# Kernel tuning notes

Measured on AMD Instinct MI355X. Metric: run time of the kernel, lower is better.

## Reference

```python
import jax, jax.numpy as jnp
import numpy as np

H = 256          # hidden_size
L = 2            # num_layers
K = 4            # khops
R = 128          # relation_num
N_NODES = 20000
N_EDGES = 160000
N_LG_EDGES = 640000


def setup_inputs() -> dict:
    key = jax.random.key(0)
    ks = iter(jax.random.split(key, 40))
    def nrm(shape, s=1.0):
        return jax.random.normal(next(ks), shape, dtype=jnp.float32) * s
    w = 1.0 / float(np.sqrt(H))
    return {
        "x": nrm((N_NODES, H)),
        "edge_feat": jax.random.randint(next(ks), (N_EDGES,), 0, R),
        "edge_index_g": jax.random.randint(next(ks), (2, N_EDGES), 0, N_NODES),
        "edge_index_lg": jax.random.randint(next(ks), (2, N_LG_EDGES), 0, N_EDGES),
        "rel_embed": nrm((R, H)),
        # per-layer, per-core (0=node update, 1=edge update) parameter stacks
        "w_self": nrm((L, 2, H, H), w), "b_self": jnp.zeros((L, 2, H), jnp.float32),
        "w_khop": nrm((L, 2, K, H, H), w), "b_khop": jnp.zeros((L, 2, K, H), jnp.float32),
        "w_fuse": nrm((L, 2, H, H), w), "b_fuse": jnp.zeros((L, 2, H), jnp.float32),
        "w_ff1": nrm((L, 2, H, 4 * H), w), "b_ff1": jnp.zeros((L, 2, 4 * H), jnp.float32),
        "w_ff2": nrm((L, 2, 4 * H, H), 1.0 / float(np.sqrt(4 * H))), "b_ff2": jnp.zeros((L, 2, H), jnp.float32),
        "ln1_g": jnp.ones((L, 2, H), jnp.float32), "ln1_b": jnp.zeros((L, 2, H), jnp.float32),
        "ln2_g": jnp.ones((L, 2, H), jnp.float32), "ln2_b": jnp.zeros((L, 2, H), jnp.float32),
    }


def _layernorm(x, g, b, eps=1e-5):
    m = jnp.mean(x, axis=-1, keepdims=True)
    v = jnp.var(x, axis=-1, keepdims=True)
    return (x - m) * jax.lax.rsqrt(v + eps) * g + b


def _core(p, src, dst, x, fused):
    """LGNNCore.forward (eval mode, dropout never applied in core)."""
    (ws, bs, wk, bk, wf, bf, w1, b1, w2, b2, g1, c1, g2, c2) = p
    n = x.shape[0]
    prev = x @ ws + bs
    # k-hop copy_src + sum aggregation, each hop gets its own linear
    z = x
    kh = jnp.zeros_like(prev)
    for i in range(wk.shape[0]):
        z = jax.ops.segment_sum(z[src], dst, num_segments=n)
        kh = kh + z @ wk[i] + bk[i]
    edge = fused @ wf + bf
    out = jax.nn.gelu(prev + kh + edge, approximate=False)
    out = _layernorm(x + out, g1, c1)
    ffn = jax.nn.gelu(out @ w1 + b1, approximate=False) @ w2 + b2
    return _layernorm(out + ffn, g2, c2)


def reference(x, edge_feat, edge_index_g, edge_index_lg, rel_embed,
              w_self, b_self, w_khop, b_khop, w_fuse, b_fuse,
              w_ff1, b_ff1, w_ff2, b_ff2, ln1_g, ln1_b, ln2_g, ln2_b):
    lg_x = rel_embed[edge_feat]                       # [n_edges, H]
    src_g, dst_g = edge_index_g[0], edge_index_g[1]
    src_l, dst_l = edge_index_lg[0], edge_index_lg[1]
    n_nodes = x.shape[0]
    for l in range(w_self.shape[0]):
        def pick(c):
            return (w_self[l, c], b_self[l, c], w_khop[l, c], b_khop[l, c],
                    w_fuse[l, c], b_fuse[l, c], w_ff1[l, c], b_ff1[l, c],
                    w_ff2[l, c], b_ff2[l, c], ln1_g[l, c], ln1_b[l, c],
                    ln2_g[l, c], ln2_b[l, c])
        # pmpd @ lg_x : scatter each edge feature to both of its endpoints
        fused_nodes = (jax.ops.segment_sum(lg_x, src_g, num_segments=n_nodes)
                       + jax.ops.segment_sum(lg_x, dst_g, num_segments=n_nodes))
        # pmpd^T @ x : gather both endpoint node features per edge
        fused_edges = x[src_g] + x[dst_g]
        new_x = _core(pick(0), src_g, dst_g, x, fused_nodes)
        new_lg_x = _core(pick(1), src_l, dst_l, lg_x, fused_edges)
        x, lg_x = new_x, new_lg_x
    return x, lg_x
```

## Files before the change

### kernel.cpp

```cpp
#include <hip/hip_runtime.h>

typedef __bf16 bf16;
typedef __attribute__((ext_vector_type(8))) __bf16 bf16x8;
typedef __attribute__((ext_vector_type(4))) __bf16 bf16x4;
typedef __attribute__((ext_vector_type(4))) float f32x4;

#define HD 256
#define GEMM_GELU 2

__device__ __forceinline__ float gelu_f(float x) {
  float x2 = x * x;
  float u = 1.5957691216057308f * x * fmaf(0.044715f, x2, 1.0f);
  float e = __expf(-u);
  return x / (1.0f + e);
}

__device__ __forceinline__ void gload_lds16(const void* g, void* l) {
  __builtin_amdgcn_global_load_lds(
      (const __attribute__((address_space(1))) unsigned int*)g,
      (__attribute__((address_space(3))) unsigned int*)l, 16, 0, 0);
}

__global__ __launch_bounds__(256) void gemm_k(
    const bf16* __restrict__ A, const bf16* __restrict__ Wt,
    const float* __restrict__ bias, bf16* __restrict__ C,
    int M, int Kd, int lda, int ldc, int flags)
{
  __shared__ __align__(16) bf16 sA[128 * 32];
  __shared__ __align__(16) bf16 sB[128 * 32];
  const int t = threadIdx.x;
  const int lane = t & 63, w = t >> 6;
  const int n0 = blockIdx.x * 128, m0 = blockIdx.y * 128;
  const int wr = w >> 1, wc = w & 1;
  const int lm = lane & 15, quad = lane >> 4;

  const int srow = t >> 2;
  const int cg = (t & 3) ^ ((t >> 3) & 3);
  const bool full = (m0 + 128 <= M);

  const char* a0 = (const char*)(A + (size_t)(m0 + srow) * lda) + cg * 16;
  const char* a1 = (const char*)(A + (size_t)(m0 + srow + 64) * lda) + cg * 16;
  const char* b0 = (const char*)(Wt + (size_t)(n0 + srow) * Kd) + cg * 16;
  const char* b1 = (const char*)(Wt + (size_t)(n0 + srow + 64) * Kd) + cg * 16;
  bf16* lA0 = sA + w * 512;
  bf16* lA1 = sA + 2048 + w * 512;
  bf16* lB0 = sB + w * 512;
  bf16* lB1 = sB + 2048 + w * 512;

  const int soff = (quad ^ ((lm >> 1) & 3)) * 8;

  f32x4 acc[4][4];
#pragma unroll
  for (int i = 0; i < 4; i++)
#pragma unroll
    for (int j = 0; j < 4; j++)
#pragma unroll
      for (int r = 0; r < 4; r++) acc[i][j][r] = 0.f;

  for (int kb = 0; kb < Kd; kb += 32) {
    size_t ko = (size_t)kb * 2;
    if (full) {
      gload_lds16(a0 + ko, lA0);
      gload_lds16(a1 + ko, lA1);
    } else {
#pragma unroll
      for (int c = 0; c < 2; c++) {
        int row = srow + c * 64;
        int gr = m0 + row;
        bf16x8 va;
#pragma unroll
        for (int q = 0; q < 8; q++) va[q] = (bf16)0.f;
        if (gr < M) va = *(const bf16x8*)((const char*)(A + (size_t)gr * lda) + ko + cg * 16);
        *(bf16x8*)(sA + row * 32 + (t & 3) * 8) = va;
      }
    }
    gload_lds16(b0 + ko, lB0);
    gload_lds16(b1 + ko, lB1);
    __syncthreads();
    bf16x8 af[4], bv[4];
#pragma unroll
    for (int i = 0; i < 4; i++) af[i] = *(const bf16x8*)(sA + (wr * 64 + i * 16 + lm) * 32 + soff);
#pragma unroll
    for (int j = 0; j < 4; j++) bv[j] = *(const bf16x8*)(sB + (wc * 64 + j * 16 + lm) * 32 + soff);
#pragma unroll
    for (int i = 0; i < 4; i++)
#pragma unroll
      for (int j = 0; j < 4; j++)
        acc[i][j] = __builtin_amdgcn_mfma_f32_16x16x32_bf16(bv[j], af[i], acc[i][j], 0, 0, 0);
    __syncthreads();
  }
#pragma unroll
  for (int i = 0; i < 4; i++) {
    int gr = m0 + wr * 64 + i * 16 + lm;
    if (gr < M) {
      bf16* crow = C + (size_t)gr * ldc;
#pragma unroll
      for (int j = 0; j < 4; j++) {
        int gc = n0 + wc * 64 + j * 16 + quad * 4;
        float4 bia = *(const float4*)(bias + gc);
        float v0 = acc[i][j][0] + bia.x;
        float v1 = acc[i][j][1] + bia.y;
        float v2 = acc[i][j][2] + bia.z;
        float v3 = acc[i][j][3] + bia.w;
        if (flags & GEMM_GELU) {
          v0 = gelu_f(v0); v1 = gelu_f(v1); v2 = gelu_f(v2); v3 = gelu_f(v3);
        }
        bf16x4 o = {(bf16)v0, (bf16)v1, (bf16)v2, (bf16)v3};
        *(bf16x4*)(crow + gc) = o;
      }
    }
  }
}

__global__ __launch_bounds__(256) void segsum_k(
    const int* __restrict__ offs, const int* __restrict__ cols,
    const bf16* __restrict__ in, int ldin, bf16* __restrict__ out, int ldout, int nseg)
{
  int wid = threadIdx.x >> 6, lane = threadIdx.x & 63;
  int seg = blockIdx.x * 4 + wid;
  if (seg >= nseg) return;
  int b = offs[seg], e = offs[seg + 1];
  float a0 = 0.f, a1 = 0.f, a2 = 0.f, a3 = 0.f;
  for (int i = b; i < e; i++) {
    int c = cols[i];
    bf16x4 v = *(const bf16x4*)(in + (size_t)c * ldin + lane * 4);
    a0 += (float)v.x; a1 += (float)v.y; a2 += (float)v.z; a3 += (float)v.w;
  }
  bf16x4 o = {(bf16)a0, (bf16)a1, (bf16)a2, (bf16)a3};
  *(bf16x4*)(out + (size_t)seg * ldout + lane * 4) = o;
}

__global__ __launch_bounds__(256) void ln_k(
    const bf16* __restrict__ X, int ldx, const bf16* __restrict__ A,
    const float* __restrict__ gam, const float* __restrict__ bet,
    bf16* __restrict__ outb, float* __restrict__ outf, int M, int apply_gelu)
{
  int wid = threadIdx.x >> 6, lane = threadIdx.x & 63;
  int row = blockIdx.x * 4 + wid;
  if (row >= M) return;
  size_t xbase = (size_t)row * ldx + lane * 4;
  size_t abase = (size_t)row * HD + lane * 4;
  bf16x4 xv = *(const bf16x4*)(X + xbase);
  bf16x4 av = *(const bf16x4*)(A + abase);
  float s0, s1, s2, s3;
  if (apply_gelu) {
    s0 = (float)xv.x + gelu_f((float)av.x);
    s1 = (float)xv.y + gelu_f((float)av.y);
    s2 = (float)xv.z + gelu_f((float)av.z);
    s3 = (float)xv.w + gelu_f((float)av.w);
  } else {
    s0 = (float)xv.x + (float)av.x;
    s1 = (float)xv.y + (float)av.y;
    s2 = (float)xv.z + (float)av.z;
    s3 = (float)xv.w + (float)av.w;
  }
  float sum = s0 + s1 + s2 + s3;
#pragma unroll
  for (int o = 32; o; o >>= 1) sum += __shfl_xor(sum, o, 64);
  float mean = sum * (1.0f / 256.0f);
  float d0 = s0 - mean, d1 = s1 - mean, d2 = s2 - mean, d3 = s3 - mean;
  float vs = d0 * d0 + d1 * d1 + d2 * d2 + d3 * d3;
#pragma unroll
  for (int o = 32; o; o >>= 1) vs += __shfl_xor(vs, o, 64);
  float rstd = rsqrtf(vs * (1.0f / 256.0f) + 1e-5f);
  float4 g = *(const float4*)(gam + lane * 4);
  float4 bb = *(const float4*)(bet + lane * 4);
  float y0 = d0 * rstd * g.x + bb.x;
  float y1 = d1 * rstd * g.y + bb.y;
  float y2 = d2 * rstd * g.z + bb.z;
  float y3 = d3 * rstd * g.w + bb.w;
  if (outb) {
    bf16x4 o = {(bf16)y0, (bf16)y1, (bf16)y2, (bf16)y3};
    *(bf16x4*)(outb + xbase) = o;
  }
  if (outf) {
    float4 o = {y0, y1, y2, y3};
    *(float4*)(outf + abase) = o;
  }
}

__global__ __launch_bounds__(256) void gather_rel_k(
    const int* __restrict__ feat, const float* __restrict__ rel,
    bf16* __restrict__ out, int ldout, int NE)
{
  int wid = threadIdx.x >> 6, lane = threadIdx.x & 63;
  int e = blockIdx.x * 4 + wid;
  if (e >= NE) return;
  int f = feat[e];
  float4 v = *(const float4*)(rel + (size_t)f * HD + lane * 4);
  bf16x4 o = {(bf16)v.x, (bf16)v.y, (bf16)v.z, (bf16)v.w};
  *(bf16x4*)(out + (size_t)e * ldout + lane * 4) = o;
}

__global__ __launch_bounds__(256) void gather2_k(
    const int* __restrict__ src, const int* __restrict__ dst,
    const bf16* __restrict__ x, int ldx, bf16* __restrict__ out, int ldout, int NE)
{
  int wid = threadIdx.x >> 6, lane = threadIdx.x & 63;
  int e = blockIdx.x * 4 + wid;
  if (e >= NE) return;
  int s = src[e], d = dst[e];
  bf16x4 a = *(const bf16x4*)(x + (size_t)s * ldx + lane * 4);
  bf16x4 b = *(const bf16x4*)(x + (size_t)d * ldx + lane * 4);
  bf16x4 o = {(bf16)((float)a.x + (float)b.x), (bf16)((float)a.y + (float)b.y),
              (bf16)((float)a.z + (float)b.z), (bf16)((float)a.w + (float)b.w)};
  *(bf16x4*)(out + (size_t)e * ldout + lane * 4) = o;
}

__global__ __launch_bounds__(256) void f2b_k(const float* __restrict__ in,
                                             bf16* __restrict__ out, int ldout, int M) {
  int wid = threadIdx.x >> 6, lane = threadIdx.x & 63;
  int row = blockIdx.x * 4 + wid;
  if (row >= M) return;
  float4 v = *(const float4*)(in + (size_t)row * HD + lane * 4);
  bf16x4 o = {(bf16)v.x, (bf16)v.y, (bf16)v.z, (bf16)v.w};
  *(bf16x4*)(out + (size_t)row * ldout + lane * 4) = o;
}

__global__ __launch_bounds__(256) void wtrans_k(const float* __restrict__ in, bf16* __restrict__ out,
                                                int Kd, int Nd) {
  size_t moff = (size_t)blockIdx.y * Kd * Nd;
  int id = blockIdx.x * 256 + threadIdx.x;
  if (id >= Kd * Nd) return;
  int n = id / Kd, k = id - n * Kd;
  out[moff + id] = (bf16)in[moff + (size_t)k * Nd + n];
}

__global__ __launch_bounds__(256) void wcat_k(const float* __restrict__ ws, const float* __restrict__ wk,
                                              const float* __restrict__ wf, bf16* __restrict__ out,
                                              int KH, int CW) {
  int mi = blockIdx.y;
  int id = blockIdx.x * 256 + threadIdx.x;
  if (id >= HD * CW) return;
  int n = id / CW, k = id - n * CW;
  int s = k >> 8, kk = k & 255;
  float v;
  if (s == 0)       v = ws[((size_t)mi * HD + kk) * HD + n];
  else if (s <= KH) v = wk[(((size_t)mi * KH + (s - 1)) * HD + kk) * HD + n];
  else              v = wf[((size_t)mi * HD + kk) * HD + n];
  out[(size_t)mi * HD * CW + id] = (bf16)v;
}

__global__ __launch_bounds__(256) void bcat_k(const float* __restrict__ bs, const float* __restrict__ bk,
                                              const float* __restrict__ bf, float* __restrict__ out, int KH) {
  int mi = blockIdx.x, n = threadIdx.x;
  float v = bs[(size_t)mi * HD + n] + bf[(size_t)mi * HD + n];
  for (int i = 0; i < KH; i++) v += bk[((size_t)mi * KH + i) * HD + n];
  out[(size_t)mi * HD + n] = v;
}

__global__ __launch_bounds__(256) void count_k(const int* __restrict__ keys, int n, int* __restrict__ cnt) {
  int i = blockIdx.x * 256 + threadIdx.x;
  if (i < n) atomicAdd(&cnt[keys[i]], 1);
}
__global__ __launch_bounds__(256) void scan1_k(const int* __restrict__ in, int* __restrict__ out,
                                               int* __restrict__ bsum, int n) {
  __shared__ int sh[256];
  int t = threadIdx.x;
  int i0 = blockIdx.x * 1024 + t * 4;
  int v0 = (i0 < n) ? in[i0] : 0;
  int v1 = (i0 + 1 < n) ? in[i0 + 1] : 0;
  int v2 = (i0 + 2 < n) ? in[i0 + 2] : 0;
  int v3 = (i0 + 3 < n) ? in[i0 + 3] : 0;
  int tsum = v0 + v1 + v2 + v3;
  sh[t] = tsum;
  __syncthreads();
  for (int o = 1; o < 256; o <<= 1) {
    int x = (t >= o) ? sh[t - o] : 0;
    __syncthreads();
    sh[t] += x;
    __syncthreads();
  }
  int e0 = sh[t] - tsum;
  if (t == 255) bsum[blockIdx.x] = sh[255];
  if (i0 < n) out[i0] = e0;
  e0 += v0;
  if (i0 + 1 < n) out[i0 + 1] = e0;
  e0 += v1;
  if (i0 + 2 < n) out[i0 + 2] = e0;
  e0 += v2;
  if (i0 + 3 < n) out[i0 + 3] = e0;
}
__global__ void scan2_k(int* bsum, int nb, int* total) {
  if (threadIdx.x == 0 && blockIdx.x == 0) {
    int acc = 0;
    for (int i = 0; i < nb; i++) { int v = bsum[i]; bsum[i] = acc; acc += v; }
    *total = acc;
  }
}
__global__ __launch_bounds__(256) void scan3_k(int* out, const int* bsum, int n) {
  int i = blockIdx.x * 256 + threadIdx.x;
  if (i < n) out[i] += bsum[i >> 10];
}
__global__ __launch_bounds__(256) void fill_k(const int* __restrict__ keys, const int* __restrict__ vals,
                                              int n, int modE, int* __restrict__ cursor, int* __restrict__ cols) {
  int i = blockIdx.x * 256 + threadIdx.x;
  if (i >= n) return;
  int pos = atomicAdd(&cursor[keys[i]], 1);
  cols[pos] = vals ? vals[i] : (i < modE ? i : i - modE);
}

extern "C" void kernel_launch(void* const* d_in, const int* in_sizes, int n_in,
                              void* d_out, int out_size, void* d_ws, size_t ws_size,
                              hipStream_t stream)
{
  const float* x_in      = (const float*)d_in[0];
  const int*   edge_feat = (const int*)d_in[1];
  const int*   eig       = (const int*)d_in[2];
  const int*   eil       = (const int*)d_in[3];
  const float* rel       = (const float*)d_in[4];
  const float* w_self = (const float*)d_in[5];
  const float* b_self = (const float*)d_in[6];
  const float* w_khop = (const float*)d_in[7];
  const float* b_khop = (const float*)d_in[8];
  const float* w_fuse = (const float*)d_in[9];
  const float* b_fuse = (const float*)d_in[10];
  const float* w_ff1  = (const float*)d_in[11];
  const float* b_ff1  = (const float*)d_in[12];
  const float* w_ff2  = (const float*)d_in[13];
  const float* b_ff2  = (const float*)d_in[14];
  const float* ln1_g  = (const float*)d_in[15];
  const float* ln1_b  = (const float*)d_in[16];
  const float* ln2_g  = (const float*)d_in[17];
  const float* ln2_b  = (const float*)d_in[18];

  const int NN = in_sizes[0] / HD;
  const int NE = in_sizes[1];
  const int NL = in_sizes[3] / 2;
  const int L  = in_sizes[5] / (2 * HD * HD);
  const int KH = in_sizes[7] / (L * 2 * HD * HD);
  const int CW = (KH + 2) * HD;

  char* p = (char*)d_ws;
  auto alloc = [&](size_t bytes) -> void* {
    void* r = (void*)p;
    p += (bytes + 255) & ~(size_t)255;
    return r;
  };

  bf16* n_cat  = (bf16*)alloc((size_t)NN * CW * 2);
  bf16* lg_cat = (bf16*)alloc((size_t)NE * CW * 2);
  bf16* acc_n  = (bf16*)alloc((size_t)NN * HD * 2);
  bf16* acc_e  = (bf16*)alloc((size_t)NE * HD * 2);

  bf16*  wcat_t = (bf16*)alloc((size_t)L * 2 * HD * CW * 2);
  float* bcat   = (float*)alloc((size_t)L * 2 * HD * 4);
  bf16*  wff1_t = (bf16*)alloc((size_t)L * 2 * HD * 4 * HD * 2);
  bf16*  wff2_t = (bf16*)alloc((size_t)L * 2 * HD * 4 * HD * 2);

  int* inc_offs = (int*)alloc((size_t)(NN + 1) * 4);
  int* inc_cur  = (int*)alloc((size_t)NN * 4);
  int* inc_cols = (int*)alloc((size_t)2 * NE * 4);
  int* ng_offs  = (int*)alloc((size_t)(NN + 1) * 4);
  int* ng_cur   = (int*)alloc((size_t)NN * 4);
  int* ng_cols  = (int*)alloc((size_t)NE * 4);
  int* lg_offs  = (int*)alloc((size_t)(NE + 1) * 4);
  int* lg_cur   = (int*)alloc((size_t)NE * 4);
  int* lg_cols  = (int*)alloc((size_t)NL * 4);
  int* bsum     = (int*)alloc(3 * 256 * 4);

  wcat_k<<<dim3((HD * CW + 255) / 256, L * 2), 256, 0, stream>>>(w_self, w_khop, w_fuse, wcat_t, KH, CW);
  bcat_k<<<L * 2, 256, 0, stream>>>(b_self, b_khop, b_fuse, bcat, KH);
  wtrans_k<<<dim3((HD * 4 * HD + 255) / 256, L * 2), 256, 0, stream>>>(w_ff1, wff1_t, HD, 4 * HD);
  wtrans_k<<<dim3((HD * 4 * HD + 255) / 256, L * 2), 256, 0, stream>>>(w_ff2, wff2_t, 4 * HD, HD);

  f2b_k<<<(NN + 3) / 4, 256, 0, stream>>>(x_in, n_cat, CW, NN);
  gather_rel_k<<<(NE + 3) / 4, 256, 0, stream>>>(edge_feat, rel, lg_cat, CW, NE);

  auto build_csr = [&](const int* keys, int nkeys, const int* vals, int modE,
                       int nseg, int* offs, int* cur, int* cols, int* bs) {
    int nb = (nseg + 1023) / 1024;
    hipMemsetAsync(offs, 0, (size_t)(nseg + 1) * 4, stream);
    count_k<<<(nkeys + 255) / 256, 256, 0, stream>>>(keys, nkeys, offs);
    scan1_k<<<nb, 256, 0, stream>>>(offs, offs, bs, nseg);
    scan2_k<<<1, 1, 0, stream>>>(bs, nb, offs + nseg);
    scan3_k<<<(nseg + 255) / 256, 256, 0, stream>>>(offs, bs, nseg);
    hipMemcpyAsync(cur, offs, (size_t)nseg * 4, hipMemcpyDeviceToDevice, stream);
    fill_k<<<(nkeys + 255) / 256, 256, 0, stream>>>(keys, vals, nkeys, modE, cur, cols);
  };
  build_csr(eig, 2 * NE, nullptr, NE, NN, inc_offs, inc_cur, inc_cols, bsum);
  build_csr(eig + NE, NE, eig, 0, NN, ng_offs, ng_cur, ng_cols, bsum + 256);
  build_csr(eil + NL, NL, eil, 0, NE, lg_offs, lg_cur, lg_cols, bsum + 512);

  float* out_x  = (float*)d_out;
  float* out_lg = (float*)d_out + (size_t)NN * HD;

  auto run_core = [&](bf16* cat, bf16* accb, const int* coffs, const int* ccols,
                      int M, int l, int c, float* outf) {
    size_t mi = (size_t)(l * 2 + c);
    int mb = (M + 127) / 128;
    for (int i = 1; i <= KH; i++)
      segsum_k<<<(M + 3) / 4, 256, 0, stream>>>(coffs, ccols, cat + (size_t)(i - 1) * HD, CW,
                                                cat + (size_t)i * HD, CW, M);
    gemm_k<<<dim3(2, mb), 256, 0, stream>>>(cat, wcat_t + mi * HD * CW, bcat + mi * HD,
                                            accb, M, CW, CW, HD, 0);
    ln_k<<<(M + 3) / 4, 256, 0, stream>>>(cat, CW, accb, ln1_g + mi * HD, ln1_b + mi * HD,
                                          cat, (float*)nullptr, M, 1);
    bf16* hid = cat + HD;
    int FC = (M > 40000) ? 40000 : M;
    for (int c0 = 0; c0 < M; c0 += FC) {
      int mc = (M - c0 < FC) ? (M - c0) : FC;
      int mbc = (mc + 127) / 128;
      gemm_k<<<dim3(8, mbc), 256, 0, stream>>>(cat + (size_t)c0 * CW, wff1_t + mi * HD * 4 * HD,
                                               b_ff1 + mi * 4 * HD, hid, mc, HD, CW, CW, GEMM_GELU);
      gemm_k<<<dim3(2, mbc), 256, 0, stream>>>(hid, wff2_t + mi * 4 * HD * HD, b_ff2 + mi * HD,
                                               accb + (size_t)c0 * HD, mc, 4 * HD, CW, HD, 0);
    }
    ln_k<<<(M + 3) / 4, 256, 0, stream>>>(cat, CW, accb, ln2_g + mi * HD, ln2_b + mi * HD,
                                          cat, outf, M, 0);
  };

  for (int l = 0; l < L; l++) {
    segsum_k<<<(NN + 3) / 4, 256, 0, stream>>>(inc_offs, inc_cols, lg_cat, CW,
                                               n_cat + (size_t)(KH + 1) * HD, CW, NN);
    gather2_k<<<(NE + 3) / 4, 256, 0, stream>>>(eig, eig + NE, n_cat, CW,
                                                lg_cat + (size_t)(KH + 1) * HD, CW, NE);
    run_core(n_cat, acc_n, ng_offs, ng_cols, NN, l, 0, (l == L - 1) ? out_x : nullptr);
    run_core(lg_cat, acc_e, lg_offs, lg_cols, NE, l, 1, (l == L - 1) ? out_lg : nullptr);
  }
}
```

Measured before the change: 3.329 ms.

## Double-buffer GEMM LDS tiles to overlap global loads with MFMA

The GEMM kernel gets two LDS buffers for A and B. The next k-tile is issued into the spare buffer while MFMAs run on the current one, so there is one barrier per iteration instead of two. Bias loads are hoisted out of the row loop in the epilogue. This doubles LDS use to 32 KB per block, which may lower occupancy, and correctness now depends on the global_load_lds writes being waited for before the barrier.

```diff
diff --git a/kernel.cpp b/kernel.cpp
--- a/kernel.cpp
+++ b/kernel.cpp
@@ -26,8 +26,8 @@
     const float* __restrict__ bias, bf16* __restrict__ C,
     int M, int Kd, int lda, int ldc, int flags)
 {
-  __shared__ __align__(16) bf16 sA[128 * 32];
-  __shared__ __align__(16) bf16 sB[128 * 32];
+  __shared__ __align__(16) bf16 sA[2][128 * 32];
+  __shared__ __align__(16) bf16 sB[2][128 * 32];
   const int t = threadIdx.x;
   const int lane = t & 63, w = t >> 6;
   const int n0 = blockIdx.x * 128, m0 = blockIdx.y * 128;
@@ -41,11 +41,7 @@
   const char* a0 = (const char*)(A + (size_t)(m0 + srow) * lda) + cg * 16;
   const char* a1 = (const char*)(A + (size_t)(m0 + srow + 64) * lda) + cg * 16;
   const char* b0 = (const char*)(Wt + (size_t)(n0 + srow) * Kd) + cg * 16;
-  const char* b1 = (const char*)(Wt + (size_t)(n0 + srow + 64) * Kd) + cg * 16;
-  bf16* lA0 = sA + w * 512;
-  bf16* lA1 = sA + 2048 + w * 512;
-  bf16* lB0 = sB + w * 512;
-  bf16* lB1 = sB + 2048 + w * 512;
+  const char* b1 = (const char*)(Wt + (size_t)(n0 + srow) * Kd) + (size_t)64 * Kd * 2 + cg * 16;
 
   const int soff = (quad ^ ((lm >> 1) & 3)) * 8;
 
@@ -57,11 +53,15 @@
 #pragma unroll
       for (int r = 0; r < 4; r++) acc[i][j][r] = 0.f;
 
-  for (int kb = 0; kb < Kd; kb += 32) {
+  const int nk = Kd >> 5;
+
+  auto stage = [&](int buf, int kb) {
     size_t ko = (size_t)kb * 2;
+    bf16* SA = sA[buf];
+    bf16* SB = sB[buf];
     if (full) {
-      gload_lds16(a0 + ko, lA0);
-      gload_lds16(a1 + ko, lA1);
+      gload_lds16(a0 + ko, SA + w * 512);
+      gload_lds16(a1 + ko, SA + 2048 + w * 512);
     } else {
 #pragma unroll
       for (int c = 0; c < 2; c++) {
@@ -71,24 +71,43 @@
 #pragma unroll
         for (int q = 0; q < 8; q++) va[q] = (bf16)0.f;
         if (gr < M) va = *(const bf16x8*)((const char*)(A + (size_t)gr * lda) + ko + cg * 16);
-        *(bf16x8*)(sA + row * 32 + (t & 3) * 8) = va;
+        *(bf16x8*)(SA + row * 32 + (t & 3) * 8) = va;
       }
     }
-    gload_lds16(b0 + ko, lB0);
-    gload_lds16(b1 + ko, lB1);
-    __syncthreads();
+    gload_lds16(b0 + ko, SB + w * 512);
+    gload_lds16(b1 + ko, SB + 2048 + w * 512);
+  };
+
+  auto compute = [&](int buf) {
+    const bf16* SA = sA[buf];
+    const bf16* SB = sB[buf];
     bf16x8 af[4], bv[4];
 #pragma unroll
-    for (int i = 0; i < 4; i++) af[i] = *(const bf16x8*)(sA + (wr * 64 + i * 16 + lm) * 32 + soff);
-#pragma unroll
-    for (int j = 0; j < 4; j++) bv[j] = *(const bf16x8*)(sB + (wc * 64 + j * 16 + lm) * 32 + soff);
+    for (int i = 0; i < 4; i++) af[i] = *(const bf16x8*)(SA + (wr * 64 + i * 16 + lm) * 32 + soff);
+#pragma unroll
+    for (int j = 0; j < 4; j++) bv[j] = *(const bf16x8*)(SB + (wc * 64 + j * 16 + lm) * 32 + soff);
 #pragma unroll
     for (int i = 0; i < 4; i++)
 #pragma unroll
       for (int j = 0; j < 4; j++)
         acc[i][j] = __builtin_amdgcn_mfma_f32_16x16x32_bf16(bv[j], af[i], acc[i][j], 0, 0, 0);
+  };
+
+  stage(0, 0);
+  __syncthreads();
+  int cur = 0;
+  for (int kt = 0; kt < nk - 1; ++kt) {
+    stage(cur ^ 1, (kt + 1) << 5);
+    compute(cur);
     __syncthreads();
-  }
+    cur ^= 1;
+  }
+  compute(cur);
+
+  float4 bia[4];
+#pragma unroll
+  for (int j = 0; j < 4; j++)
+    bia[j] = *(const float4*)(bias + n0 + wc * 64 + j * 16 + quad * 4);
 #pragma unroll
   for (int i = 0; i < 4; i++) {
     int gr = m0 + wr * 64 + i * 16 + lm;
@@ -97,11 +116,10 @@
 #pragma unroll
       for (int j = 0; j < 4; j++) {
         int gc = n0 + wc * 64 + j * 16 + quad * 4;
-        float4 bia = *(const float4*)(bias + gc);
-        float v0 = acc[i][j][0] + bia.x;
-        float v1 = acc[i][j][1] + bia.y;
-        float v2 = acc[i][j][2] + bia.z;
-        float v3 = acc[i][j][3] + bia.w;
+        float v0 = acc[i][j][0] + bia[j].x;
+        float v1 = acc[i][j][1] + bia[j].y;
+        float v2 = acc[i][j][2] + bia[j].z;
+        float v3 = acc[i][j][3] + bia[j].w;
         if (flags & GEMM_GELU) {
           v0 = gelu_f(v0); v1 = gelu_f(v1); v2 = gelu_f(v2); v3 = gelu_f(v3);
         }
```

Result: no change. 3.268 ms (-1.8%).
